# Kernel tuning notes

Measured on AMD Instinct MI355X. Metric: run time of the kernel, lower is better.

The kernel has to match this reference:

```python
import jax, jax.numpy as jnp
import numpy as np

N_NODES = 100000
N_EDGES = 3200000
IN_F, H1, H2, N_CLS = 128, 64, 64, 4


def setup_inputs() -> dict:
    key = jax.random.key(0)
    ks = jax.random.split(key, 8)
    x = jax.random.normal(ks[0], (N_NODES, IN_F), dtype=jnp.float32)
    edge_index = jax.random.randint(ks[1], (2, N_EDGES), 0, N_NODES, dtype=jnp.int32)
    def glorot(k, fan_in, fan_out):
        lim = (6.0 / (fan_in + fan_out)) ** 0.5
        return jax.random.uniform(k, (fan_in, fan_out), jnp.float32, -lim, lim)
    return {
        'x': x,
        'edge_index': edge_index,
        'W1': glorot(ks[2], IN_F, H1), 'b1': jnp.zeros((H1,), jnp.float32),
        'W2': glorot(ks[3], H1, H2),  'b2': jnp.zeros((H2,), jnp.float32),
        'W3': glorot(ks[4], H2, N_CLS), 'b3': jnp.zeros((N_CLS,), jnp.float32),
    }


def gcn_conv(x, row, col, W, b, n_nodes):
    # symmetric normalization D^{-1/2} (A+I) D^{-1/2}, self-loops already in row/col
    deg = jax.ops.segment_sum(jnp.ones_like(col, dtype=x.dtype), col, num_segments=n_nodes)
    dis = jnp.where(deg > 0, jax.lax.rsqrt(jnp.maximum(deg, 1.0)), 0.0)
    norm = dis[row] * dis[col]            # [E']
    h = x @ W                              # [N, out]
    msg = h[row] * norm[:, None]           # gather + scale  [E', out]
    out = jax.ops.segment_sum(msg, col, num_segments=n_nodes)  # scatter-add
    return out + b


def reference(x, edge_index, W1, b1, W2, b2, W3, b3):
    n = x.shape[0]
    loop = jnp.arange(n, dtype=edge_index.dtype)
    row = jnp.concatenate([edge_index[0], loop])
    col = jnp.concatenate([edge_index[1], loop])
    h = gcn_conv(x, row, col, W1, b1, n)
    h = jax.nn.relu(h)
    # dropout p=0.5 is identity in eval mode
    h = gcn_conv(h, row, col, W2, b2, n)
    out = gcn_conv(h, row, col, W3, b3, n)
    return out
```

## Files before the change

kernel.cpp:

```cpp
#include <hip/hip_runtime.h>

#define IN_F 128
#define H 64

#define BKT_BITS 8
#define BKT_SZ 256
#define NBKT_MAX 512
#define CHUNK 8192

using half8 = __attribute__((ext_vector_type(8))) _Float16;
using half2v = __attribute__((ext_vector_type(2))) _Float16;
using f32x4 = __attribute__((ext_vector_type(4))) float;


__global__ void p1_bucket_count(const int* __restrict__ col, int* __restrict__ bucketCnt,
                                int E, int nbkt) {
    __shared__ int h[NBKT_MAX];
    int t = threadIdx.x;
    for (int i = t; i < NBKT_MAX; i += 256) h[i] = 0;
    __syncthreads();
    int beg = blockIdx.x * CHUNK;
    int end = min(E, beg + CHUNK);
    for (int j = beg + t; j < end; j += 256)
        atomicAdd(&h[col[j] >> BKT_BITS], 1);
    __syncthreads();
    for (int i = t; i < nbkt; i += 256)
        if (h[i]) atomicAdd(&bucketCnt[i], h[i]);
}


__global__ void p2_bucket_scan(const int* __restrict__ bucketCnt, int* __restrict__ base,
                               int* __restrict__ cursor, int nbkt) {
    __shared__ int s[NBKT_MAX];
    int t = threadIdx.x;
    int v = (t < nbkt) ? bucketCnt[t] : 0;
    s[t] = v;
    __syncthreads();
    for (int off = 1; off < NBKT_MAX; off <<= 1) {
        int tmp = (t >= off) ? s[t - off] : 0;
        __syncthreads();
        s[t] += tmp;
        __syncthreads();
    }
    if (t < nbkt) {
        int b = s[t] - v;
        base[t] = b;
        cursor[t] = b;
    }
    if (t == nbkt - 1) base[nbkt] = s[t];
}


__global__ void p3_partition(const int* __restrict__ row, const int* __restrict__ col,
                             int* __restrict__ cursor, int2* __restrict__ part,
                             int E, int nbkt) {
    __shared__ int h[NBKT_MAX];
    __shared__ int res[NBKT_MAX];
    int t = threadIdx.x;
    for (int i = t; i < NBKT_MAX; i += 256) h[i] = 0;
    __syncthreads();
    int beg = blockIdx.x * CHUNK;
    int end = min(E, beg + CHUNK);
    for (int j = beg + t; j < end; j += 256)
        atomicAdd(&h[col[j] >> BKT_BITS], 1);
    __syncthreads();
    for (int i = t; i < nbkt; i += 256) {
        int c = h[i];
        res[i] = c ? atomicAdd(&cursor[i], c) : 0;
    }
    __syncthreads();
    for (int i = t; i < NBKT_MAX; i += 256) h[i] = 0;
    __syncthreads();
    for (int j = beg + t; j < end; j += 256) {
        int c = col[j];
        int b = c >> BKT_BITS;
        int l = atomicAdd(&h[b], 1);
        int2 pr; pr.x = row[j]; pr.y = c;
        part[res[b] + l] = pr;
    }
}


__global__ void p4_csr(const int2* __restrict__ part, const int* __restrict__ base,
                       int* __restrict__ offs, int* __restrict__ srcb,
                       float* __restrict__ dis, int N, int nbkt) {
    __shared__ int deg[BKT_SZ];
    __shared__ int lofs[BKT_SZ];
    __shared__ int cur[BKT_SZ];
    int b = blockIdx.x, t = threadIdx.x;
    int eb = base[b], ee = base[b + 1];
    deg[t] = 0;
    __syncthreads();
    for (int j = eb + t; j < ee; j += 256)
        atomicAdd(&deg[part[j].y & (BKT_SZ - 1)], 1);
    __syncthreads();
    int v = deg[t];
    lofs[t] = v;
    __syncthreads();
    for (int off = 1; off < BKT_SZ; off <<= 1) {
        int tmp = (t >= off) ? lofs[t - off] : 0;
        __syncthreads();
        lofs[t] += tmp;
        __syncthreads();
    }
    int excl = lofs[t] - v;
    int g = (b << BKT_BITS) + t;
    if (g < N) {
        offs[g] = eb + excl;
        dis[g] = rsqrtf((float)(v + 1));
    }
    if (b == nbkt - 1 && t == 0) offs[N] = ee;
    deg[t] = excl;
    cur[t] = 0;
    __syncthreads();
    for (int j = eb + t; j < ee; j += 256) {
        int2 pr = part[j];
        int loc = pr.y & (BKT_SZ - 1);
        int l = atomicAdd(&cur[loc], 1);
        srcb[eb + deg[loc] + l] = pr.x;
    }
}


__global__ void prep_w(const float* __restrict__ W1, const float* __restrict__ W2,
                       _Float16* __restrict__ WT1, _Float16* __restrict__ WT2) {
    int t = blockIdx.x * 256 + threadIdx.x;
    int stride = gridDim.x * 256;
    for (int i = t; i < IN_F * H; i += stride) {
        int k = i >> 6, c = i & 63;
        WT1[c * IN_F + k] = (_Float16)W1[i];
    }
    for (int i = t; i < H * H; i += stride) {
        int k = i >> 6, c = i & 63;
        WT2[c * H + k] = (_Float16)W2[i];
    }
}


__global__ __launch_bounds__(256) void mm1_mfma(const float* __restrict__ x,
                                                const _Float16* __restrict__ WT1,
                                                const float* __restrict__ dis,
                                                _Float16* __restrict__ out, int N) {
    int t = threadIdx.x;
    int w = t >> 6, l = t & 63, lr = l & 15, lg = l >> 4;
    int r0 = blockIdx.x * 64 + w * 16;
    if (r0 >= N) return;
    half8 bfrag[4][4];
#pragma unroll
    for (int ct = 0; ct < 4; ++ct)
#pragma unroll
        for (int ks = 0; ks < 4; ++ks)
            bfrag[ct][ks] = *(const half8*)(WT1 + (size_t)(ct * 16 + lr) * IN_F + ks * 32 + lg * 8);
    int ar = min(r0 + lr, N - 1);
    const float* ap = x + (size_t)ar * IN_F + lg * 8;
    f32x4 acc0 = {0.f, 0.f, 0.f, 0.f}, acc1 = acc0, acc2 = acc0, acc3 = acc0;
#pragma unroll
    for (int ks = 0; ks < 4; ++ks) {
        float4 a0 = *(const float4*)(ap + ks * 32);
        float4 a1 = *(const float4*)(ap + ks * 32 + 4);
        half8 a;
        a[0] = (_Float16)a0.x; a[1] = (_Float16)a0.y; a[2] = (_Float16)a0.z; a[3] = (_Float16)a0.w;
        a[4] = (_Float16)a1.x; a[5] = (_Float16)a1.y; a[6] = (_Float16)a1.z; a[7] = (_Float16)a1.w;
        acc0 = __builtin_amdgcn_mfma_f32_16x16x32_f16(a, bfrag[0][ks], acc0, 0, 0, 0);
        acc1 = __builtin_amdgcn_mfma_f32_16x16x32_f16(a, bfrag[1][ks], acc1, 0, 0, 0);
        acc2 = __builtin_amdgcn_mfma_f32_16x16x32_f16(a, bfrag[2][ks], acc2, 0, 0, 0);
        acc3 = __builtin_amdgcn_mfma_f32_16x16x32_f16(a, bfrag[3][ks], acc3, 0, 0, 0);
    }
#pragma unroll
    for (int reg = 0; reg < 4; ++reg) {
        int r = r0 + lg * 4 + reg;
        if (r < N) {
            float d = dis[r];
            _Float16* o = out + (size_t)r * H + lr;
            o[0]  = (_Float16)(d * acc0[reg]);
            o[16] = (_Float16)(d * acc1[reg]);
            o[32] = (_Float16)(d * acc2[reg]);
            o[48] = (_Float16)(d * acc3[reg]);
        }
    }
}

__global__ __launch_bounds__(256) void mm2_mfma(const _Float16* __restrict__ hh,
                                                const float* __restrict__ b1,
                                                const _Float16* __restrict__ WT2,
                                                const float* __restrict__ dis,
                                                _Float16* __restrict__ out, int N) {
    int t = threadIdx.x;
    int w = t >> 6, l = t & 63, lr = l & 15, lg = l >> 4;
    int r0 = blockIdx.x * 64 + w * 16;
    if (r0 >= N) return;
    half8 bfrag[4][2];
#pragma unroll
    for (int ct = 0; ct < 4; ++ct)
#pragma unroll
        for (int ks = 0; ks < 2; ++ks)
            bfrag[ct][ks] = *(const half8*)(WT2 + (size_t)(ct * 16 + lr) * H + ks * 32 + lg * 8);
    float bias0[8], bias1[8];
#pragma unroll
    for (int j = 0; j < 8; ++j) bias0[j] = b1[lg * 8 + j];
#pragma unroll
    for (int j = 0; j < 8; ++j) bias1[j] = b1[32 + lg * 8 + j];
    int ar = min(r0 + lr, N - 1);
    const _Float16* ap = hh + (size_t)ar * H + lg * 8;
    f32x4 acc0 = {0.f, 0.f, 0.f, 0.f}, acc1 = acc0, acc2 = acc0, acc3 = acc0;
#pragma unroll
    for (int ks = 0; ks < 2; ++ks) {
        half8 a = *(const half8*)(ap + ks * 32);
        half8 af;
#pragma unroll
        for (int j = 0; j < 8; ++j) {
            float v = (float)a[j] + (ks ? bias1[j] : bias0[j]);
            af[j] = (_Float16)fmaxf(v, 0.f);
        }
        acc0 = __builtin_amdgcn_mfma_f32_16x16x32_f16(af, bfrag[0][ks], acc0, 0, 0, 0);
        acc1 = __builtin_amdgcn_mfma_f32_16x16x32_f16(af, bfrag[1][ks], acc1, 0, 0, 0);
        acc2 = __builtin_amdgcn_mfma_f32_16x16x32_f16(af, bfrag[2][ks], acc2, 0, 0, 0);
        acc3 = __builtin_amdgcn_mfma_f32_16x16x32_f16(af, bfrag[3][ks], acc3, 0, 0, 0);
    }
#pragma unroll
    for (int reg = 0; reg < 4; ++reg) {
        int r = r0 + lg * 4 + reg;
        if (r < N) {
            float d = dis[r];
            _Float16* o = out + (size_t)r * H + lr;
            o[0]  = (_Float16)(d * acc0[reg]);
            o[16] = (_Float16)(d * acc1[reg]);
            o[32] = (_Float16)(d * acc2[reg]);
            o[48] = (_Float16)(d * acc3[reg]);
        }
    }
}

__global__ void mm3(const _Float16* __restrict__ hh, const float* __restrict__ b,
                    const float* __restrict__ W, const float* __restrict__ dis,
                    float* __restrict__ out, int N) {
    __shared__ float Wl[H * 4];
    __shared__ float bl[H];
    int t = threadIdx.x;
    if (t < H * 4) Wl[t] = W[t];
    if (t < H) bl[t] = b[t];
    __syncthreads();
    int c = t & 3, rr = t >> 2;
    int r = blockIdx.x * 64 + rr;
    if (r >= N) return;
    const _Float16* h0 = hh + (size_t)r * H;
    float a = 0;
    for (int k = 0; k < H; k += 8) {
        half8 v = *(const half8*)(h0 + k);
#pragma unroll
        for (int j = 0; j < 8; ++j)
            a += ((float)v[j] + bl[k + j]) * Wl[(k + j) * 4 + c];
    }
    out[(size_t)r * 4 + c] = dis[r] * a;
}


__global__ void agg64h(const _Float16* __restrict__ xs, const int* __restrict__ offs,
                       const int* __restrict__ src, const float* __restrict__ dis,
                       _Float16* __restrict__ out, int N) {
    int wid = (blockIdx.x * 256 + threadIdx.x) >> 6;
    int lane = threadIdx.x & 63;
    if (wid >= N) return;
    int es = lane >> 5;
    int f2 = lane & 31;
    int beg = offs[wid], end = offs[wid + 1];
    const _Float16* base = xs + (size_t)f2 * 2;
    float ax = 0.f, ay = 0.f;
    int j = beg + es;
    for (; j + 14 < end; j += 16) {
        int s0 = src[j],      s1 = src[j + 2],  s2 = src[j + 4],  s3 = src[j + 6];
        int s4 = src[j + 8],  s5 = src[j + 10], s6 = src[j + 12], s7 = src[j + 14];
        half2v v0 = *(const half2v*)(base + (size_t)s0 * 64);
        half2v v1 = *(const half2v*)(base + (size_t)s1 * 64);
        half2v v2 = *(const half2v*)(base + (size_t)s2 * 64);
        half2v v3 = *(const half2v*)(base + (size_t)s3 * 64);
        half2v v4 = *(const half2v*)(base + (size_t)s4 * 64);
        half2v v5 = *(const half2v*)(base + (size_t)s5 * 64);
        half2v v6 = *(const half2v*)(base + (size_t)s6 * 64);
        half2v v7 = *(const half2v*)(base + (size_t)s7 * 64);
        ax += (float)v0[0]; ay += (float)v0[1];
        ax += (float)v1[0]; ay += (float)v1[1];
        ax += (float)v2[0]; ay += (float)v2[1];
        ax += (float)v3[0]; ay += (float)v3[1];
        ax += (float)v4[0]; ay += (float)v4[1];
        ax += (float)v5[0]; ay += (float)v5[1];
        ax += (float)v6[0]; ay += (float)v6[1];
        ax += (float)v7[0]; ay += (float)v7[1];
    }
    for (; j < end; j += 2) {
        half2v v = *(const half2v*)(base + (size_t)src[j] * 64);
        ax += (float)v[0]; ay += (float)v[1];
    }
    ax += __shfl_xor(ax, 32);
    ay += __shfl_xor(ay, 32);
    if (es == 0) {
        half2v sv = *(const half2v*)(base + (size_t)wid * 64);
        float d = dis[wid];
        half2v o;
        o[0] = (_Float16)(d * ((float)sv[0] + ax));
        o[1] = (_Float16)(d * ((float)sv[1] + ay));
        *(half2v*)(out + (size_t)wid * 64 + f2 * 2) = o;
    }
}

__global__ void agg4(const float* __restrict__ xs, const int* __restrict__ offs,
                     const int* __restrict__ src, const float* __restrict__ dis,
                     const float* __restrict__ b, float* __restrict__ out, int N) {
    int i = blockIdx.x * 256 + threadIdx.x;
    if (i >= N) return;
    float4 v = *(const float4*)(xs + (size_t)i * 4);
    float4 acc = v;
    int beg = offs[i], end = offs[i + 1];
    for (int j = beg; j < end; ++j) {
        float4 m = *(const float4*)(xs + (size_t)src[j] * 4);
        acc.x += m.x; acc.y += m.y; acc.z += m.z; acc.w += m.w;
    }
    float d = dis[i];
    float4 o;
    o.x = b[0] + d * acc.x;
    o.y = b[1] + d * acc.y;
    o.z = b[2] + d * acc.z;
    o.w = b[3] + d * acc.w;
    *(float4*)(out + (size_t)i * 4) = o;
}


extern "C" void kernel_launch(void* const* d_in, const int* in_sizes, int n_in,
                              void* d_out, int out_size, void* d_ws, size_t ws_size,
                              hipStream_t stream) {
    const float* x  = (const float*)d_in[0];
    const int*   ei = (const int*)d_in[1];
    const float* W1 = (const float*)d_in[2];
    const float* b1 = (const float*)d_in[3];
    const float* W2 = (const float*)d_in[4];
    const float* b2 = (const float*)d_in[5];
    const float* W3 = (const float*)d_in[6];
    const float* b3 = (const float*)d_in[7];
    float* out = (float*)d_out;
    (void)n_in; (void)out_size; (void)ws_size;

    const int N = in_sizes[0] / IN_F;
    const int E = in_sizes[1] / 2;
    const int* row = ei;
    const int* col = ei + E;
    const int nbkt = (N + BKT_SZ - 1) >> BKT_BITS;

    char* w = (char*)d_ws;
    auto carve = [&](size_t bytes) { char* p = w; w += (bytes + 255) & ~(size_t)255; return p; };
    _Float16* bufX  = (_Float16*)carve((size_t)N * H * 2);
    _Float16* bufY  = (_Float16*)carve((size_t)N * H * 2);
    _Float16* WT1   = (_Float16*)carve((size_t)IN_F * H * 2);
    _Float16* WT2   = (_Float16*)carve((size_t)H * H * 2);
    float*  bufC   = (float*)carve((size_t)N * 4 * 4);
    float*  dis    = (float*)carve((size_t)N * 4);
    int*    offs   = (int*)carve((size_t)(N + 1) * 4);
    int*    srcb   = (int*)carve((size_t)E * 4);
    int2*   part   = (int2*)carve((size_t)E * 8);
    int*    bktCnt = (int*)carve((size_t)NBKT_MAX * 4);
    int*    bktBas = (int*)carve((size_t)(NBKT_MAX + 1) * 4);
    int*    bktCur = (int*)carve((size_t)NBKT_MAX * 4);

    (void)hipMemsetAsync(bktCnt, 0, (size_t)nbkt * 4, stream);

    int gE = (E + CHUNK - 1) / CHUNK;
    int gN = (N + 255) / 256;
    int gMM = (N + 63) / 64;

    p1_bucket_count<<<gE, 256, 0, stream>>>(col, bktCnt, E, nbkt);
    p2_bucket_scan<<<1, NBKT_MAX, 0, stream>>>(bktCnt, bktBas, bktCur, nbkt);
    p3_partition<<<gE, 256, 0, stream>>>(row, col, bktCur, part, E, nbkt);
    p4_csr<<<nbkt, BKT_SZ, 0, stream>>>(part, bktBas, offs, srcb, dis, N, nbkt);

    prep_w<<<48, 256, 0, stream>>>(W1, W2, WT1, WT2);

    mm1_mfma<<<gMM, 256, 0, stream>>>(x, WT1, dis, bufX, N);
    agg64h<<<(N + 3) / 4, 256, 0, stream>>>(bufX, offs, srcb, dis, bufY, N);
    mm2_mfma<<<gMM, 256, 0, stream>>>(bufY, b1, WT2, dis, bufX, N);
    agg64h<<<(N + 3) / 4, 256, 0, stream>>>(bufX, offs, srcb, dis, bufY, N);
    mm3<<<gMM, 256, 0, stream>>>(bufY, b2, W3, dis, bufC, N);
    agg4<<<gN, 256, 0, stream>>>(bufC, offs, srcb, dis, b3, out, N);
}
```

Measured before the change: 331.1 us.

## Pack partition entries into 32 bits and widen aggregation gathers

The partition buffer now stores each edge as one 32-bit word: the source row sits in the low 24 bits and the local destination index within the 256-node bucket in the high 8 bits. This halves the write and read traffic between the partition and CSR-building passes. The 64-wide fp16 aggregation now has each lane load 4 halves (8 bytes) instead of 2, with four edge streams per wavefront. Source indices are fetched 32 at a time with one coalesced load and broadcast via shuffles. The 4-wide aggregation loop is unrolled by four to keep more gathers in flight. Packing assumes node ids fit in 24 bits.

```diff
diff --git a/kernel.cpp b/kernel.cpp
--- a/kernel.cpp
+++ b/kernel.cpp
@@ -9,7 +9,7 @@
 #define CHUNK 8192
 
 using half8 = __attribute__((ext_vector_type(8))) _Float16;
-using half2v = __attribute__((ext_vector_type(2))) _Float16;
+using half4 = __attribute__((ext_vector_type(4))) _Float16;
 using f32x4 = __attribute__((ext_vector_type(4))) float;
 
 
@@ -52,7 +52,7 @@
 
 
 __global__ void p3_partition(const int* __restrict__ row, const int* __restrict__ col,
-                             int* __restrict__ cursor, int2* __restrict__ part,
+                             int* __restrict__ cursor, int* __restrict__ part,
                              int E, int nbkt) {
     __shared__ int h[NBKT_MAX];
     __shared__ int res[NBKT_MAX];
@@ -75,13 +75,13 @@
         int c = col[j];
         int b = c >> BKT_BITS;
         int l = atomicAdd(&h[b], 1);
-        int2 pr; pr.x = row[j]; pr.y = c;
-        part[res[b] + l] = pr;
-    }
-}
-
-
-__global__ void p4_csr(const int2* __restrict__ part, const int* __restrict__ base,
+        int pk = (int)(((unsigned)(c & (BKT_SZ - 1)) << 24) | (unsigned)row[j]);
+        part[res[b] + l] = pk;
+    }
+}
+
+
+__global__ void p4_csr(const int* __restrict__ part, const int* __restrict__ base,
                        int* __restrict__ offs, int* __restrict__ srcb,
                        float* __restrict__ dis, int N, int nbkt) {
     __shared__ int deg[BKT_SZ];
@@ -92,7 +92,7 @@
     deg[t] = 0;
     __syncthreads();
     for (int j = eb + t; j < ee; j += 256)
-        atomicAdd(&deg[part[j].y & (BKT_SZ - 1)], 1);
+        atomicAdd(&deg[(unsigned)part[j] >> 24], 1);
     __syncthreads();
     int v = deg[t];
     lofs[t] = v;
@@ -114,10 +114,10 @@
     cur[t] = 0;
     __syncthreads();
     for (int j = eb + t; j < ee; j += 256) {
-        int2 pr = part[j];
-        int loc = pr.y & (BKT_SZ - 1);
+        int pk = part[j];
+        int loc = (unsigned)pk >> 24;
         int l = atomicAdd(&cur[loc], 1);
-        srcb[eb + deg[loc] + l] = pr.x;
+        srcb[eb + deg[loc] + l] = pk & 0xFFFFFF;
     }
 }
 
@@ -261,45 +261,41 @@
     int wid = (blockIdx.x * 256 + threadIdx.x) >> 6;
     int lane = threadIdx.x & 63;
     if (wid >= N) return;
-    int es = lane >> 5;
-    int f2 = lane & 31;
+    int s = lane >> 4;
+    int f = lane & 15;
     int beg = offs[wid], end = offs[wid + 1];
-    const _Float16* base = xs + (size_t)f2 * 2;
-    float ax = 0.f, ay = 0.f;
-    int j = beg + es;
-    for (; j + 14 < end; j += 16) {
-        int s0 = src[j],      s1 = src[j + 2],  s2 = src[j + 4],  s3 = src[j + 6];
-        int s4 = src[j + 8],  s5 = src[j + 10], s6 = src[j + 12], s7 = src[j + 14];
-        half2v v0 = *(const half2v*)(base + (size_t)s0 * 64);
-        half2v v1 = *(const half2v*)(base + (size_t)s1 * 64);
-        half2v v2 = *(const half2v*)(base + (size_t)s2 * 64);
-        half2v v3 = *(const half2v*)(base + (size_t)s3 * 64);
-        half2v v4 = *(const half2v*)(base + (size_t)s4 * 64);
-        half2v v5 = *(const half2v*)(base + (size_t)s5 * 64);
-        half2v v6 = *(const half2v*)(base + (size_t)s6 * 64);
-        half2v v7 = *(const half2v*)(base + (size_t)s7 * 64);
-        ax += (float)v0[0]; ay += (float)v0[1];
-        ax += (float)v1[0]; ay += (float)v1[1];
-        ax += (float)v2[0]; ay += (float)v2[1];
-        ax += (float)v3[0]; ay += (float)v3[1];
-        ax += (float)v4[0]; ay += (float)v4[1];
-        ax += (float)v5[0]; ay += (float)v5[1];
-        ax += (float)v6[0]; ay += (float)v6[1];
-        ax += (float)v7[0]; ay += (float)v7[1];
-    }
-    for (; j < end; j += 2) {
-        half2v v = *(const half2v*)(base + (size_t)src[j] * 64);
-        ax += (float)v[0]; ay += (float)v[1];
-    }
-    ax += __shfl_xor(ax, 32);
-    ay += __shfl_xor(ay, 32);
-    if (es == 0) {
-        half2v sv = *(const half2v*)(base + (size_t)wid * 64);
+    int deg = end - beg;
+    const _Float16* base = xs + (size_t)f * 4;
+    float a0 = 0.f, a1 = 0.f, a2 = 0.f, a3 = 0.f;
+    int nfull = deg >> 5;
+    int j = beg;
+    for (int it = 0; it < nfull; ++it, j += 32) {
+        int idx = src[j + (lane & 31)];
+#pragma unroll
+        for (int k = 0; k < 8; ++k) {
+            int sk = __shfl(idx, s * 8 + k);
+            half4 v = *(const half4*)(base + (size_t)sk * 64);
+            a0 += (float)v[0]; a1 += (float)v[1]; a2 += (float)v[2]; a3 += (float)v[3];
+        }
+    }
+    for (int jj = j + s; jj < end; jj += 4) {
+        int sk = src[jj];
+        half4 v = *(const half4*)(base + (size_t)sk * 64);
+        a0 += (float)v[0]; a1 += (float)v[1]; a2 += (float)v[2]; a3 += (float)v[3];
+    }
+    a0 += __shfl_xor(a0, 16); a0 += __shfl_xor(a0, 32);
+    a1 += __shfl_xor(a1, 16); a1 += __shfl_xor(a1, 32);
+    a2 += __shfl_xor(a2, 16); a2 += __shfl_xor(a2, 32);
+    a3 += __shfl_xor(a3, 16); a3 += __shfl_xor(a3, 32);
+    if (s == 0) {
+        half4 sv = *(const half4*)(base + (size_t)wid * 64);
         float d = dis[wid];
-        half2v o;
-        o[0] = (_Float16)(d * ((float)sv[0] + ax));
-        o[1] = (_Float16)(d * ((float)sv[1] + ay));
-        *(half2v*)(out + (size_t)wid * 64 + f2 * 2) = o;
+        half4 o;
+        o[0] = (_Float16)(d * ((float)sv[0] + a0));
+        o[1] = (_Float16)(d * ((float)sv[1] + a1));
+        o[2] = (_Float16)(d * ((float)sv[2] + a2));
+        o[3] = (_Float16)(d * ((float)sv[3] + a3));
+        *(half4*)(out + (size_t)wid * 64 + f * 4) = o;
     }
 }
 
@@ -311,7 +307,19 @@
     float4 v = *(const float4*)(xs + (size_t)i * 4);
     float4 acc = v;
     int beg = offs[i], end = offs[i + 1];
-    for (int j = beg; j < end; ++j) {
+    int j = beg;
+    for (; j + 3 < end; j += 4) {
+        int s0 = src[j], s1 = src[j + 1], s2 = src[j + 2], s3 = src[j + 3];
+        float4 m0 = *(const float4*)(xs + (size_t)s0 * 4);
+        float4 m1 = *(const float4*)(xs + (size_t)s1 * 4);
+        float4 m2 = *(const float4*)(xs + (size_t)s2 * 4);
+        float4 m3 = *(const float4*)(xs + (size_t)s3 * 4);
+        acc.x += m0.x + m1.x + m2.x + m3.x;
+        acc.y += m0.y + m1.y + m2.y + m3.y;
+        acc.z += m0.z + m1.z + m2.z + m3.z;
+        acc.w += m0.w + m1.w + m2.w + m3.w;
+    }
+    for (; j < end; ++j) {
         float4 m = *(const float4*)(xs + (size_t)src[j] * 4);
         acc.x += m.x; acc.y += m.y; acc.z += m.z; acc.w += m.w;
     }
@@ -355,7 +363,7 @@
     float*  dis    = (float*)carve((size_t)N * 4);
     int*    offs   = (int*)carve((size_t)(N + 1) * 4);
     int*    srcb   = (int*)carve((size_t)E * 4);
-    int2*   part   = (int2*)carve((size_t)E * 8);
+    int*    part   = (int*)carve((size_t)E * 4);
     int*    bktCnt = (int*)carve((size_t)NBKT_MAX * 4);
     int*    bktBas = (int*)carve((size_t)(NBKT_MAX + 1) * 4);
     int*    bktCur = (int*)carve((size_t)NBKT_MAX * 4);
```

Measured after the change: 310.9 us. 1.07x faster.
